# Optimization experiments

Measured on AMD Instinct MI355X. Metric: run time of the kernel, lower is better.

Reference implementation:

```python
import jax, jax.numpy as jnp
import numpy as np

N, E, DIN, DH, DOUT = 50000, 800000, 256, 128, 64


def setup_inputs() -> dict:
    key = jax.random.key(0)
    ks = jax.random.split(key, 12)
    return {
        "h": jax.random.normal(ks[0], (N, DIN), jnp.float32),
        "src": jax.random.randint(ks[1], (E,), 0, N, jnp.int32),
        "dst": jax.random.randint(ks[2], (E,), 0, N, jnp.int32),
        "W1": jax.random.normal(ks[3], (DIN, DH), jnp.float32) * (DIN ** -0.5),
        "al1": jax.random.normal(ks[4], (DH,), jnp.float32) * (DH ** -0.5),
        "ar1": jax.random.normal(ks[5], (DH,), jnp.float32) * (DH ** -0.5),
        "W2": jax.random.normal(ks[6], (DH, DH), jnp.float32) * (DH ** -0.5),
        "al2": jax.random.normal(ks[7], (DH,), jnp.float32) * (DH ** -0.5),
        "ar2": jax.random.normal(ks[8], (DH,), jnp.float32) * (DH ** -0.5),
        "W3": jax.random.normal(ks[9], (DH, DOUT), jnp.float32) * (DH ** -0.5),
        "al3": jax.random.normal(ks[10], (DOUT,), jnp.float32) * (DOUT ** -0.5),
        "ar3": jax.random.normal(ks[11], (DOUT,), jnp.float32) * (DOUT ** -0.5),
    }


def gat_layer(h, W, al, ar, src, dst):
    """DGL GATConv, 1 head, no bias: proj -> leaky_relu edge scores -> edge softmax over dst -> scatter-sum."""
    n = h.shape[0]
    f = h @ W                                   # [N, d]
    el = f @ al                                 # [N]
    er = f @ ar                                 # [N]
    e = jax.nn.leaky_relu(el[src] + er[dst], negative_slope=0.2)  # [E]
    m = jax.ops.segment_max(e, dst, num_segments=n)
    m = jnp.where(jnp.isfinite(m), m, 0.0)      # zero-in-degree nodes
    m = jax.lax.stop_gradient(m)
    ex = jnp.exp(e - m[dst])                    # [E]
    z = jax.ops.segment_sum(ex, dst, num_segments=n)
    a = ex / jnp.maximum(z, 1e-9)[dst]          # [E] softmax weights
    return jax.ops.segment_sum(a[:, None] * f[src], dst, num_segments=n)


def reference(h, src, dst, W1, al1, ar1, W2, al2, ar2, W3, al3, ar3):
    x = gat_layer(h, W1, al1, ar1, src, dst)
    x = jax.nn.relu(x)                          # dropout = identity (eval)
    x = gat_layer(x, W2, al2, ar2, src, dst)
    x = jax.nn.relu(x)
    x = gat_layer(x, W3, al3, ar3, src, dst)    # mean over 1 head = identity
    return jax.nn.log_softmax(x, axis=-1)
```

## Files before the change

### kernel.cpp

```cpp
#include <hip/hip_runtime.h>
#include <math.h>

#define DIN 256
#define DHID 128
#define DOUTC 64
#define EPB 2048

typedef __attribute__((ext_vector_type(8))) short short8;
typedef __attribute__((ext_vector_type(4))) float f32x4;

static __device__ __forceinline__ float wave_max(float v){
  #pragma unroll
  for (int o=1;o<64;o<<=1) v = fmaxf(v, __shfl_xor(v,o,64));
  return v;
}
static __device__ __forceinline__ float wave_sum(float v){
  #pragma unroll
  for (int o=1;o<64;o<<=1) v += __shfl_xor(v,o,64);
  return v;
}

static __device__ __forceinline__ unsigned short bf16_rne(float x){
  unsigned int u = __float_as_uint(x);
  return (unsigned short)((u + 0x7FFFu + ((u>>16)&1u)) >> 16);
}
static __device__ __forceinline__ float bf16_to_f32(unsigned short h){
  return __uint_as_float(((unsigned int)h)<<16);
}
static __device__ __forceinline__ float blo(unsigned int u){ return __uint_as_float(u<<16); }
static __device__ __forceinline__ float bhi(unsigned int u){ return __uint_as_float(u & 0xffff0000u); }

__global__ __launch_bounds__(256) void rs_hist(const int* __restrict__ dst,
    int* __restrict__ ghist, int E, int NB){
  __shared__ int h[256];
  const int t = threadIdx.x, blk = blockIdx.x;
  h[t] = 0; __syncthreads();
  const int base = blk*EPB;
  #pragma unroll
  for (int i=0;i<EPB/256;i++){
    int j = base + i*256 + t;
    if (j < E) atomicAdd(&h[dst[j]>>8], 1);
  }
  __syncthreads();
  ghist[t*NB + blk] = h[t];
}

__global__ __launch_bounds__(256) void rs_scan(int* __restrict__ ghist,
    int* __restrict__ btot, int NB){
  __shared__ int b[256];
  __shared__ int carry;
  const int hb = blockIdx.x, t = threadIdx.x;
  if (t==0) carry = 0;
  __syncthreads();
  for (int c0=0; c0<NB; c0+=256){
    int i = c0 + t;
    int v = (i<NB)? ghist[hb*NB+i] : 0;
    b[t] = v; __syncthreads();
    #pragma unroll
    for (int o=1;o<256;o<<=1){
      int x = (t>=o)? b[t-o] : 0;
      __syncthreads();
      b[t] += x;
      __syncthreads();
    }
    if (i<NB) ghist[hb*NB+i] = carry + b[t] - v;
    __syncthreads();
    if (t==255) carry += b[255];
    __syncthreads();
  }
  if (t==255) btot[hb] = carry;
}

__global__ __launch_bounds__(256) void rs_scan2(int* __restrict__ btot,
    int* __restrict__ offsets, int N, int E){
  __shared__ int b[256];
  const int t = threadIdx.x;
  int v = btot[t];
  b[t] = v; __syncthreads();
  #pragma unroll
  for (int o=1;o<256;o<<=1){
    int x = (t>=o)? b[t-o] : 0;
    __syncthreads();
    b[t] += x;
    __syncthreads();
  }
  btot[t] = b[t] - v;
  if (t==255){ btot[256] = E; offsets[N] = E; }
}

__global__ __launch_bounds__(256) void rs_scatter(const int* __restrict__ src,
    const int* __restrict__ dst, const int* __restrict__ ghist,
    const int* __restrict__ btot, uint2* __restrict__ ebuf, int E, int NB){
  __shared__ int cur[256];
  const int t = threadIdx.x, blk = blockIdx.x;
  cur[t] = ghist[t*NB + blk] + btot[t];
  __syncthreads();
  const int base = blk*EPB;
  #pragma unroll
  for (int i=0;i<EPB/256;i++){
    int j = base + i*256 + t;
    if (j < E){
      int d = dst[j];
      int pos = atomicAdd(&cur[d>>8], 1);
      ebuf[pos] = make_uint2((unsigned)src[j], (unsigned)d);
    }
  }
}

__global__ __launch_bounds__(256) void bucket_sort(const uint2* __restrict__ ebuf,
    const int* __restrict__ btot, int* __restrict__ offsets,
    int* __restrict__ srcs, int N){
  __shared__ int h[256];
  __shared__ int b[256];
  const int hb = blockIdx.x, t = threadIdx.x;
  const int b0 = btot[hb], b1 = btot[hb+1];
  h[t] = 0; __syncthreads();
  for (int j=b0+t; j<b1; j+=256) atomicAdd(&h[ebuf[j].y & 255u], 1);
  __syncthreads();
  int v = h[t];
  b[t] = v; __syncthreads();
  #pragma unroll
  for (int o=1;o<256;o<<=1){
    int x = (t>=o)? b[t-o] : 0;
    __syncthreads();
    b[t] += x;
    __syncthreads();
  }
  const int excl = b[t] - v;
  const int node = hb*256 + t;
  if (node < N) offsets[node] = b0 + excl;
  h[t] = excl;
  __syncthreads();
  for (int j=b0+t; j<b1; j+=256){
    uint2 e = ebuf[j];
    int pos = b0 + atomicAdd(&h[e.y & 255u], 1);
    srcs[pos] = (int)e.x;
  }
}

template<int K, int NC>
__global__ void pack_kernel(const float* __restrict__ W, unsigned short* __restrict__ Wp){
  constexpr int CT = NC/16, KT = K/32;
  int idx = blockIdx.x*256 + threadIdx.x;
  if (idx >= KT*CT*64) return;
  int l = idx & 63, t = idx >> 6;
  int ct = t % CT, kt = t / CT;
  int col = ct*16 + (l & 15);
  int k0 = kt*32 + (l >> 4)*8;
  unsigned short* dstp = Wp + (size_t)idx*16;
  #pragma unroll
  for (int j=0;j<8;j++){
    float x = W[(size_t)(k0+j)*NC + col];
    unsigned short h = bf16_rne(x);
    dstp[j] = h;
    dstp[8+j] = bf16_rne(x - bf16_to_f32(h));
  }
}

template<int K, int NC>
__global__ __launch_bounds__(256) void gemm_mfma(const float* __restrict__ A,
    const unsigned short* __restrict__ Wp,
    const float* __restrict__ al, const float* __restrict__ ar,
    unsigned short* __restrict__ Fb, float* __restrict__ el, float* __restrict__ er, int nrows)
{
  constexpr int CT = NC/16, KT = K/32;
  const int lane = threadIdx.x & 63;
  const int wid  = threadIdx.x >> 6;
  const int row0 = blockIdx.x*64 + wid*16;
  const int c = lane & 15, g = lane >> 4;
  const int arow = row0 + c;
  const bool aok = arow < nrows;

  f32x4 acc[CT];
  #pragma unroll
  for (int i=0;i<CT;i++) acc[i] = (f32x4)0.f;

  #pragma unroll
  for (int kt=0; kt<KT; ++kt){
    const int k0 = kt*32 + g*8;
    float xs[8];
    if (aok){
      float4 v0 = *(const float4*)&A[(size_t)arow*K + k0];
      float4 v1 = *(const float4*)&A[(size_t)arow*K + k0 + 4];
      xs[0]=v0.x; xs[1]=v0.y; xs[2]=v0.z; xs[3]=v0.w;
      xs[4]=v1.x; xs[5]=v1.y; xs[6]=v1.z; xs[7]=v1.w;
    } else {
      #pragma unroll
      for (int j=0;j<8;j++) xs[j]=0.f;
    }
    short8 ahi, alo;
    #pragma unroll
    for (int j=0;j<8;j++){
      unsigned short h = bf16_rne(xs[j]);
      ahi[j] = (short)h;
      alo[j] = (short)bf16_rne(xs[j] - bf16_to_f32(h));
    }
    #pragma unroll
    for (int ct=0; ct<CT; ++ct){
      const size_t base = ((size_t)((kt*CT+ct)*64 + lane))*16;
      short8 bhi8 = *(const short8*)&Wp[base];
      short8 blo8 = *(const short8*)&Wp[base+8];
      acc[ct] = __builtin_amdgcn_mfma_f32_16x16x32_bf16(ahi, bhi8, acc[ct], 0,0,0);
      acc[ct] = __builtin_amdgcn_mfma_f32_16x16x32_bf16(alo, bhi8, acc[ct], 0,0,0);
      acc[ct] = __builtin_amdgcn_mfma_f32_16x16x32_bf16(ahi, blo8, acc[ct], 0,0,0);
    }
  }

  float alv[CT], arv[CT];
  #pragma unroll
  for (int ct=0;ct<CT;ct++){ alv[ct]=al[ct*16+c]; arv[ct]=ar[ct*16+c]; }
  #pragma unroll
  for (int j=0;j<4;j++){
    const int row = row0 + g*4 + j;
    const bool ok = row < nrows;
    float sl=0.f, sr=0.f;
    #pragma unroll
    for (int ct=0;ct<CT;ct++){
      float f = acc[ct][j];
      sl = fmaf(f, alv[ct], sl);
      sr = fmaf(f, arv[ct], sr);
      if (ok) Fb[(size_t)row*NC + ct*16 + c] = bf16_rne(f);
    }
    #pragma unroll
    for (int o=1;o<16;o<<=1){ sl += __shfl_xor(sl,o,64); sr += __shfl_xor(sr,o,64); }
    if (ok && c==0){ el[row]=sl; er[row]=sr; }
  }
}

template<int D, bool RELU, bool LOGSM>
__global__ __launch_bounds__(256) void agg3_kernel(const unsigned short* __restrict__ Fb,
    const float* __restrict__ el, const float* __restrict__ er,
    const int* __restrict__ offsets, const int* __restrict__ srcs,
    float* __restrict__ out, int N)
{
  constexpr int CPL = D/16;
  __shared__ float2 ws[4][64];
  const int wv = threadIdx.x >> 6;
  const int lane = threadIdx.x & 63;
  const int c16 = lane & 15, g = lane >> 4;
  const int v = blockIdx.x*4 + wv;
  if (v >= N) return;
  const int o0 = offsets[v], o1 = offsets[v+1];
  const float erv = er[v];

  float m = -INFINITY, z = 0.f;
  float acc[CPL];
  #pragma unroll
  for (int i=0;i<CPL;i++) acc[i]=0.f;

  for (int s0 = o0; s0 < o1; s0 += 64){
    const int j = s0 + lane;
    int sidx = 0; float e = -INFINITY;
    if (j < o1){
      sidx = srcs[j];
      float tv = el[sidx] + erv;
      e = (tv > 0.f) ? tv : 0.2f*tv;
    }
    const float nm = fmaxf(m, wave_max(e));
    const float scale = __expf(m - nm);
    const float wgt = __expf(e - nm);
    z = z*scale + wave_sum(wgt);
    #pragma unroll
    for (int i=0;i<CPL;i++) acc[i] *= scale;
    m = nm;
    ws[wv][lane] = make_float2(wgt, __int_as_float(sidx));
    __builtin_amdgcn_wave_barrier();

    const int cnt = min(64, o1 - s0);
    int t = g;
    if (D == 128){
      for (; t+4 < cnt; t += 8){
        float2 p0 = ws[wv][t], p1 = ws[wv][t+4];
        uint4 u0 = *((const uint4*)(Fb + (size_t)__float_as_int(p0.y)*128) + c16);
        uint4 u1 = *((const uint4*)(Fb + (size_t)__float_as_int(p1.y)*128) + c16);
        acc[0]=fmaf(p0.x, blo(u0.x), acc[0]); acc[1]=fmaf(p0.x, bhi(u0.x), acc[1]);
        acc[2]=fmaf(p0.x, blo(u0.y), acc[2]); acc[3]=fmaf(p0.x, bhi(u0.y), acc[3]);
        acc[4]=fmaf(p0.x, blo(u0.z), acc[4]); acc[5]=fmaf(p0.x, bhi(u0.z), acc[5]);
        acc[6]=fmaf(p0.x, blo(u0.w), acc[6]); acc[7]=fmaf(p0.x, bhi(u0.w), acc[7]);
        acc[0]=fmaf(p1.x, blo(u1.x), acc[0]); acc[1]=fmaf(p1.x, bhi(u1.x), acc[1]);
        acc[2]=fmaf(p1.x, blo(u1.y), acc[2]); acc[3]=fmaf(p1.x, bhi(u1.y), acc[3]);
        acc[4]=fmaf(p1.x, blo(u1.z), acc[4]); acc[5]=fmaf(p1.x, bhi(u1.z), acc[5]);
        acc[6]=fmaf(p1.x, blo(u1.w), acc[6]); acc[7]=fmaf(p1.x, bhi(u1.w), acc[7]);
      }
      if (t < cnt){
        float2 p0 = ws[wv][t];
        uint4 u0 = *((const uint4*)(Fb + (size_t)__float_as_int(p0.y)*128) + c16);
        acc[0]=fmaf(p0.x, blo(u0.x), acc[0]); acc[1]=fmaf(p0.x, bhi(u0.x), acc[1]);
        acc[2]=fmaf(p0.x, blo(u0.y), acc[2]); acc[3]=fmaf(p0.x, bhi(u0.y), acc[3]);
        acc[4]=fmaf(p0.x, blo(u0.z), acc[4]); acc[5]=fmaf(p0.x, bhi(u0.z), acc[5]);
        acc[6]=fmaf(p0.x, blo(u0.w), acc[6]); acc[7]=fmaf(p0.x, bhi(u0.w), acc[7]);
      }
    } else {
      for (; t+4 < cnt; t += 8){
        float2 p0 = ws[wv][t], p1 = ws[wv][t+4];
        uint2 u0 = *((const uint2*)(Fb + (size_t)__float_as_int(p0.y)*64) + c16);
        uint2 u1 = *((const uint2*)(Fb + (size_t)__float_as_int(p1.y)*64) + c16);
        acc[0]=fmaf(p0.x, blo(u0.x), acc[0]); acc[1]=fmaf(p0.x, bhi(u0.x), acc[1]);
        acc[2]=fmaf(p0.x, blo(u0.y), acc[2]); acc[3]=fmaf(p0.x, bhi(u0.y), acc[3]);
        acc[0]=fmaf(p1.x, blo(u1.x), acc[0]); acc[1]=fmaf(p1.x, bhi(u1.x), acc[1]);
        acc[2]=fmaf(p1.x, blo(u1.y), acc[2]); acc[3]=fmaf(p1.x, bhi(u1.y), acc[3]);
      }
      if (t < cnt){
        float2 p0 = ws[wv][t];
        uint2 u0 = *((const uint2*)(Fb + (size_t)__float_as_int(p0.y)*64) + c16);
        acc[0]=fmaf(p0.x, blo(u0.x), acc[0]); acc[1]=fmaf(p0.x, bhi(u0.x), acc[1]);
        acc[2]=fmaf(p0.x, blo(u0.y), acc[2]); acc[3]=fmaf(p0.x, bhi(u0.y), acc[3]);
      }
    }
    __builtin_amdgcn_wave_barrier();
  }

  #pragma unroll
  for (int i=0;i<CPL;i++){
    acc[i] += __shfl_xor(acc[i],16,64);
    acc[i] += __shfl_xor(acc[i],32,64);
  }
  const float zi = 1.f / fmaxf(z, 1e-9f);

  if (LOGSM){
    float y[CPL];
    #pragma unroll
    for (int i=0;i<CPL;i++) y[i] = acc[i]*zi;
    float M = y[0];
    #pragma unroll
    for (int i=1;i<CPL;i++) M = fmaxf(M, y[i]);
    #pragma unroll
    for (int o=1;o<16;o<<=1) M = fmaxf(M, __shfl_xor(M,o,64));
    float ssum = 0.f;
    #pragma unroll
    for (int i=0;i<CPL;i++) ssum += __expf(y[i]-M);
    #pragma unroll
    for (int o=1;o<16;o<<=1) ssum += __shfl_xor(ssum,o,64);
    const float lw = M + logf(ssum);
    if (g==0){
      float4 r = make_float4(y[0]-lw, y[1]-lw, y[2]-lw, y[3]-lw);
      *(float4*)&out[(size_t)v*64 + c16*4] = r;
    }
  } else {
    if (g==0){
      float r[CPL];
      #pragma unroll
      for (int i=0;i<CPL;i++){ r[i]=acc[i]*zi; if (RELU) r[i]=fmaxf(r[i],0.f); }
      *(float4*)&out[(size_t)v*128 + c16*8]     = make_float4(r[0],r[1],r[2],r[3]);
      *(float4*)&out[(size_t)v*128 + c16*8 + 4] = make_float4(r[4],r[5],r[6],r[7]);
    }
  }
}

extern "C" void kernel_launch(void* const* d_in, const int* in_sizes, int n_in,
                              void* d_out, int out_size, void* d_ws, size_t ws_size,
                              hipStream_t stream) {
  const float* h   = (const float*)d_in[0];
  const int*   src = (const int*)d_in[1];
  const int*   dst = (const int*)d_in[2];
  const float* W1  = (const float*)d_in[3];
  const float* al1 = (const float*)d_in[4];
  const float* ar1 = (const float*)d_in[5];
  const float* W2  = (const float*)d_in[6];
  const float* al2 = (const float*)d_in[7];
  const float* ar2 = (const float*)d_in[8];
  const float* W3  = (const float*)d_in[9];
  const float* al3 = (const float*)d_in[10];
  const float* ar3 = (const float*)d_in[11];

  const int N = in_sizes[0] / DIN;
  const int E = in_sizes[1];
  const int NB = (E + EPB - 1) / EPB;
  const int NHB = (N + 255) / 256;

  auto alignup = [](size_t x){ return (x + 255) & ~(size_t)255; };
  char* p = (char*)d_ws;
  int* offsets = (int*)p; p += alignup(((size_t)N+1)*4);
  int* srcs    = (int*)p; p += alignup((size_t)E*4);
  int* ghist   = (int*)p; p += alignup((size_t)256*NB*4);
  int* btot    = (int*)p; p += alignup(257*4);
  uint2* ebuf  = (uint2*)p; p += alignup((size_t)E*8);
  unsigned short* Fb = (unsigned short*)p; p += alignup((size_t)N*DHID*2);
  float* X     = (float*)p; p += alignup((size_t)N*DHID*4);
  float* el    = (float*)p; p += alignup((size_t)N*4);
  float* er    = (float*)p; p += alignup((size_t)N*4);
  unsigned short* Wp1 = (unsigned short*)p; p += alignup((size_t)2*DIN*DHID*2);
  unsigned short* Wp2 = (unsigned short*)p; p += alignup((size_t)2*DHID*DHID*2);
  unsigned short* Wp3 = (unsigned short*)p; p += alignup((size_t)2*DHID*DOUTC*2);

  const int nbW4 = (N+3)/4;
  const int nbG  = (N+63)/64;

  pack_kernel<DIN ,DHID ><<<(DIN/32)*(DHID/16)*64/256,  256,0,stream>>>(W1, Wp1);
  pack_kernel<DHID,DHID ><<<(DHID/32)*(DHID/16)*64/256, 256,0,stream>>>(W2, Wp2);
  pack_kernel<DHID,DOUTC><<<(DHID/32)*(DOUTC/16)*64/256,256,0,stream>>>(W3, Wp3);

  rs_hist   <<<NB, 256,0,stream>>>(dst, ghist, E, NB);
  rs_scan   <<<256,256,0,stream>>>(ghist, btot, NB);
  rs_scan2  <<<1,  256,0,stream>>>(btot, offsets, N, E);
  rs_scatter<<<NB, 256,0,stream>>>(src, dst, ghist, btot, ebuf, E, NB);
  bucket_sort<<<NHB,256,0,stream>>>(ebuf, btot, offsets, srcs, N);

  gemm_mfma<DIN,DHID><<<nbG,256,0,stream>>>(h, Wp1, al1, ar1, Fb, el, er, N);
  agg3_kernel<128,true,false><<<nbW4,256,0,stream>>>(Fb, el, er, offsets, srcs, X, N);

  gemm_mfma<DHID,DHID><<<nbG,256,0,stream>>>(X, Wp2, al2, ar2, Fb, el, er, N);
  agg3_kernel<128,true,false><<<nbW4,256,0,stream>>>(Fb, el, er, offsets, srcs, X, N);

  gemm_mfma<DHID,DOUTC><<<nbG,256,0,stream>>>(X, Wp3, al3, ar3, Fb, el, er, N);
  agg3_kernel<64,false,true><<<nbW4,256,0,stream>>>(Fb, el, er, offsets, srcs, (float*)d_out, N);
}
```

Measured before the change: 202.2 us.

## Stage packed weights in LDS and drop low-bf16 weight term in GEMM

The GEMM now copies the packed bf16 weight tiles into shared memory in chunks, so each block shares them instead of every wave reading them from global memory. The weight packing keeps only the high bf16 part, which halves the packed-weight footprint and removes one of the three MFMAs per tile. This trades some accuracy for less work, since weights become plain bf16 while activations keep the hi/lo split. It also adds __syncthreads barriers and LDS traffic for each chunk.

```diff
diff --git a/kernel.cpp b/kernel.cpp
--- a/kernel.cpp
+++ b/kernel.cpp
@@ -147,25 +147,27 @@
   int ct = t % CT, kt = t / CT;
   int col = ct*16 + (l & 15);
   int k0 = kt*32 + (l >> 4)*8;
-  unsigned short* dstp = Wp + (size_t)idx*16;
-  #pragma unroll
-  for (int j=0;j<8;j++){
-    float x = W[(size_t)(k0+j)*NC + col];
-    unsigned short h = bf16_rne(x);
-    dstp[j] = h;
-    dstp[8+j] = bf16_rne(x - bf16_to_f32(h));
-  }
+  unsigned short* dstp = Wp + (size_t)idx*8;
+  #pragma unroll
+  for (int j=0;j<8;j++)
+    dstp[j] = bf16_rne(W[(size_t)(k0+j)*NC + col]);
 }
 
 template<int K, int NC>
-__global__ __launch_bounds__(256) void gemm_mfma(const float* __restrict__ A,
+__global__ __launch_bounds__(256) void gemm_v3(const float* __restrict__ A,
     const unsigned short* __restrict__ Wp,
     const float* __restrict__ al, const float* __restrict__ ar,
     unsigned short* __restrict__ Fb, float* __restrict__ el, float* __restrict__ er, int nrows)
 {
   constexpr int CT = NC/16, KT = K/32;
-  const int lane = threadIdx.x & 63;
-  const int wid  = threadIdx.x >> 6;
+  constexpr int CHUNK_KT = (32/CT) < KT ? (32/CT) : KT;
+  constexpr int NCHUNK = KT / CHUNK_KT;
+  constexpr int CHUNK_SHORTS = CHUNK_KT*CT*64*8;
+  __shared__ unsigned short bsm[CHUNK_SHORTS];
+
+  const int tid = threadIdx.x;
+  const int lane = tid & 63;
+  const int wid  = tid >> 6;
   const int row0 = blockIdx.x*64 + wid*16;
   const int c = lane & 15, g = lane >> 4;
   const int arow = row0 + c;
@@ -175,34 +177,43 @@
   #pragma unroll
   for (int i=0;i<CT;i++) acc[i] = (f32x4)0.f;
 
-  #pragma unroll
-  for (int kt=0; kt<KT; ++kt){
-    const int k0 = kt*32 + g*8;
-    float xs[8];
-    if (aok){
-      float4 v0 = *(const float4*)&A[(size_t)arow*K + k0];
-      float4 v1 = *(const float4*)&A[(size_t)arow*K + k0 + 4];
-      xs[0]=v0.x; xs[1]=v0.y; xs[2]=v0.z; xs[3]=v0.w;
-      xs[4]=v1.x; xs[5]=v1.y; xs[6]=v1.z; xs[7]=v1.w;
-    } else {
+  for (int ch=0; ch<NCHUNK; ++ch){
+    if (ch) __syncthreads();
+    {
+      const uint4* gsrc = (const uint4*)Wp + (size_t)ch*(CHUNK_SHORTS/8);
+      uint4* ldst = (uint4*)bsm;
       #pragma unroll
-      for (int j=0;j<8;j++) xs[j]=0.f;
-    }
-    short8 ahi, alo;
-    #pragma unroll
-    for (int j=0;j<8;j++){
-      unsigned short h = bf16_rne(xs[j]);
-      ahi[j] = (short)h;
-      alo[j] = (short)bf16_rne(xs[j] - bf16_to_f32(h));
-    }
-    #pragma unroll
-    for (int ct=0; ct<CT; ++ct){
-      const size_t base = ((size_t)((kt*CT+ct)*64 + lane))*16;
-      short8 bhi8 = *(const short8*)&Wp[base];
-      short8 blo8 = *(const short8*)&Wp[base+8];
-      acc[ct] = __builtin_amdgcn_mfma_f32_16x16x32_bf16(ahi, bhi8, acc[ct], 0,0,0);
-      acc[ct] = __builtin_amdgcn_mfma_f32_16x16x32_bf16(alo, bhi8, acc[ct], 0,0,0);
-      acc[ct] = __builtin_amdgcn_mfma_f32_16x16x32_bf16(ahi, blo8, acc[ct], 0,0,0);
+      for (int i=0; i<CHUNK_SHORTS/8/256; ++i)
+        ldst[i*256 + tid] = gsrc[i*256 + tid];
+    }
+    __syncthreads();
+
+    #pragma unroll
+    for (int ktl=0; ktl<CHUNK_KT; ++ktl){
+      const int k0 = (ch*CHUNK_KT + ktl)*32 + g*8;
+      float xs[8];
+      if (aok){
+        float4 v0 = *(const float4*)&A[(size_t)arow*K + k0];
+        float4 v1 = *(const float4*)&A[(size_t)arow*K + k0 + 4];
+        xs[0]=v0.x; xs[1]=v0.y; xs[2]=v0.z; xs[3]=v0.w;
+        xs[4]=v1.x; xs[5]=v1.y; xs[6]=v1.z; xs[7]=v1.w;
+      } else {
+        #pragma unroll
+        for (int j=0;j<8;j++) xs[j]=0.f;
+      }
+      short8 ahi, alo;
+      #pragma unroll
+      for (int j=0;j<8;j++){
+        unsigned short hh = bf16_rne(xs[j]);
+        ahi[j] = (short)hh;
+        alo[j] = (short)bf16_rne(xs[j] - bf16_to_f32(hh));
+      }
+      #pragma unroll
+      for (int ct=0; ct<CT; ++ct){
+        short8 b = *(const short8*)&bsm[(ktl*CT+ct)*512 + lane*8];
+        acc[ct] = __builtin_amdgcn_mfma_f32_16x16x32_bf16(ahi, b, acc[ct], 0,0,0);
+        acc[ct] = __builtin_amdgcn_mfma_f32_16x16x32_bf16(alo, b, acc[ct], 0,0,0);
+      }
     }
   }
 
@@ -379,9 +390,9 @@
   float* X     = (float*)p; p += alignup((size_t)N*DHID*4);
   float* el    = (float*)p; p += alignup((size_t)N*4);
   float* er    = (float*)p; p += alignup((size_t)N*4);
-  unsigned short* Wp1 = (unsigned short*)p; p += alignup((size_t)2*DIN*DHID*2);
-  unsigned short* Wp2 = (unsigned short*)p; p += alignup((size_t)2*DHID*DHID*2);
-  unsigned short* Wp3 = (unsigned short*)p; p += alignup((size_t)2*DHID*DOUTC*2);
+  unsigned short* Wp1 = (unsigned short*)p; p += alignup((size_t)(DIN/32)*(DHID/16)*64*8*2);
+  unsigned short* Wp2 = (unsigned short*)p; p += alignup((size_t)(DHID/32)*(DHID/16)*64*8*2);
+  unsigned short* Wp3 = (unsigned short*)p; p += alignup((size_t)(DHID/32)*(DOUTC/16)*64*8*2);
 
   const int nbW4 = (N+3)/4;
   const int nbG  = (N+63)/64;
@@ -396,12 +407,12 @@
   rs_scatter<<<NB, 256,0,stream>>>(src, dst, ghist, btot, ebuf, E, NB);
   bucket_sort<<<NHB,256,0,stream>>>(ebuf, btot, offsets, srcs, N);
 
-  gemm_mfma<DIN,DHID><<<nbG,256,0,stream>>>(h, Wp1, al1, ar1, Fb, el, er, N);
+  gemm_v3<DIN,DHID><<<nbG,256,0,stream>>>(h, Wp1, al1, ar1, Fb, el, er, N);
   agg3_kernel<128,true,false><<<nbW4,256,0,stream>>>(Fb, el, er, offsets, srcs, X, N);
 
-  gemm_mfma<DHID,DHID><<<nbG,256,0,stream>>>(X, Wp2, al2, ar2, Fb, el, er, N);
+  gemm_v3<DHID,DHID><<<nbG,256,0,stream>>>(X, Wp2, al2, ar2, Fb, el, er, N);
   agg3_kernel<128,true,false><<<nbW4,256,0,stream>>>(Fb, el, er, offsets, srcs, X, N);
 
-  gemm_mfma<DHID,DOUTC><<<nbG,256,0,stream>>>(X, Wp3, al3, ar3, Fb, el, er, N);
+  gemm_v3<DHID,DOUTC><<<nbG,256,0,stream>>>(X, Wp3, al3, ar3, Fb, el, er, N);
   agg3_kernel<64,false,true><<<nbW4,256,0,stream>>>(Fb, el, er, offsets, srcs, (float*)d_out, N);
 }
```

After: 180.3 us. 10.8% less time.
